# Kernel optimization log

Measured on AMD Instinct MI355X. Metric: run time of the kernel, lower is better.

Reference implementation:

```python
import jax, jax.numpy as jnp
import numpy as np

B, T, C, K, V = 4, 2048, 1024, 1024, 1024
SQRT_K = float(np.sqrt(K))


def setup_inputs() -> dict:
    key = jax.random.key(0)
    ks = jax.random.split(key, 7)
    s = 0.02
    return {
        "x": jax.random.normal(ks[0], (B, T, C), jnp.float32),
        "Wq": (jax.random.normal(ks[1], (C, K), jnp.float32) * s),
        "bq": jnp.zeros((K,), jnp.float32),
        "Wk": (jax.random.normal(ks[2], (C, K), jnp.float32) * s),
        "bk": jnp.zeros((K,), jnp.float32),
        "Wv": (jax.random.normal(ks[3], (C, V), jnp.float32) * s),
        "bv": jnp.zeros((V,), jnp.float32),
    }


def reference(x, Wq, bq, Wk, bk, Wv, bv):
    # projections: [B,T,C] @ [C,K] -> [B,T,K]
    q = x @ Wq + bq
    k = x @ Wk + bk
    v = x @ Wv + bv
    # logits[b,t,s] = q[b,t,:] . k[b,s,:]
    logits = jnp.einsum("btk,bsk->bts", q, k)
    # original mask: mask[j,i] = 1 if i > j -> strict upper triangle masked to -inf
    seq = logits.shape[1]
    mask = jnp.triu(jnp.ones((seq, seq), bool), k=1)
    logits = jnp.where(mask[None, :, :], -jnp.inf, logits)
    # NOTE: original softmax is over dim=1 (query axis), not the key axis
    probs = jax.nn.softmax(logits / SQRT_K, axis=1)
    read = jnp.einsum("bts,bsv->btv", probs, v)
    return jnp.concatenate((x, read), axis=2)
```

## Files before the change

### kernel.cpp

```cpp
#include <hip/hip_runtime.h>
#include <hip/hip_bf16.h>
#include <stdint.h>

#define DEVI __device__ __forceinline__

using u16 = unsigned short;
typedef __attribute__((ext_vector_type(8))) _Float16 halfx8;
typedef __attribute__((ext_vector_type(4))) float f32x4;

constexpr int BB = 4, TT = 2048, CC = 1024, KD = 1024, VD = 1024;
constexpr int QKVW = 3072;
constexpr int OUTW = CC + VD;
constexpr float INV_SQRT_K = 0.03125f;

DEVI u16 f2h(float f) {
  _Float16 h = (_Float16)f;
  return __builtin_bit_cast(u16, h);
}
DEVI float h2f(u16 u) {
  return (float)__builtin_bit_cast(_Float16, u);
}

DEVI void gload16(const u16* g, u16* l) {
  __builtin_amdgcn_global_load_lds(
      (const __attribute__((address_space(1))) void*)g,
      (__attribute__((address_space(3))) void*)l, 16, 0, 0);
}

__global__ void cast_x_copy(const float* __restrict__ x, u16* __restrict__ xh,
                            float* __restrict__ out) {
  size_t i = (size_t)blockIdx.x * blockDim.x + threadIdx.x;
  float4 v = reinterpret_cast<const float4*>(x)[i];
  ushort4 u;
  u.x = f2h(v.x); u.y = f2h(v.y); u.z = f2h(v.z); u.w = f2h(v.w);
  reinterpret_cast<ushort4*>(xh)[i] = u;
  size_t e = i * 4;
  size_t bt = e / CC;
  int c = (int)(e % CC);
  *reinterpret_cast<float4*>(&out[bt * OUTW + c]) = v;
}

__global__ void transpose_cast_w3(const float* __restrict__ Wq,
                                  const float* __restrict__ Wk,
                                  const float* __restrict__ Wv,
                                  u16* __restrict__ Wt) {
  __shared__ float tile[32][33];
  const float* W = (blockIdx.z == 0) ? Wq : (blockIdx.z == 1) ? Wk : Wv;
  u16* dst = Wt + (size_t)blockIdx.z * 1024 * 1024;
  int n0 = blockIdx.x * 32, c0 = blockIdx.y * 32;
  int tx = threadIdx.x, ty = threadIdx.y;
  for (int i = ty; i < 32; i += 8)
    tile[i][tx] = W[(size_t)(c0 + i) * KD + n0 + tx];
  __syncthreads();
  for (int i = ty; i < 32; i += 8)
    dst[(size_t)(n0 + i) * CC + c0 + tx] = f2h(tile[tx][i]);
}

__global__ void concat_bias(const float* __restrict__ bq, const float* __restrict__ bk,
                            const float* __restrict__ bv, float* __restrict__ bc) {
  int n = blockIdx.x * 256 + threadIdx.x;
  float v = (n < 1024) ? bq[n] : (n < 2048) ? bk[n - 1024] : bv[n - 2048];
  bc[n] = v;
}

__global__ void transpose_v(const u16* __restrict__ QKV, const float* __restrict__ Dp,
                            u16* __restrict__ Vt) {
  __shared__ u16 tile[32][33];
  int b = blockIdx.z;
  int n0 = blockIdx.x * 32, s0 = blockIdx.y * 32;
  const u16* src = QKV + (size_t)b * TT * QKVW + 2048;
  u16* dst = Vt + (size_t)b * VD * TT;
  int tx = threadIdx.x, ty = threadIdx.y;
  for (int i = ty; i < 32; i += 8)
    tile[i][tx] = src[(size_t)(s0 + i) * QKVW + n0 + tx];
  const int s = s0 + tx;
  float d = 0.f;
  for (int rt = s >> 8; rt < TT / 256; ++rt)
    d += Dp[((size_t)rt * BB + b) * TT + s];
  float di = 1.f / d;
  __syncthreads();
  for (int i = ty; i < 32; i += 8)
    dst[(size_t)(n0 + i) * TT + s0 + tx] = f2h(h2f(tile[tx][i]) * di);
}

template <typename OutT, int TPB, int BM, int BN, int SWZ, bool CSKIP, bool KLIM,
          bool BIAS, bool CMASK>
__global__ __launch_bounds__(TPB, 2) void gemm_bt(
    const u16* __restrict__ A, const u16* __restrict__ Bm, OutT* __restrict__ Out,
    const float* __restrict__ bias, float* __restrict__ Dp,
    int Kd, int lda, int ldb, int ldo,
    long long strA, long long strB, long long strO, float alpha) {
  constexpr int BK = 32;
  constexpr int WAVES = TPB / 64;
  constexpr int WM = BM / 64, WN = WAVES / WM;
  constexpr int WR = 64, WC = 64;
  constexpr int MR = 4, NR = 4;
  constexpr int RPS = TPB / 4;
  constexpr int SWA = BM / RPS, SWB = BN / RPS;
  constexpr int LPT = SWA + SWB;
  constexpr int ASZ = BM * BK, BSZ = BN * BK;
  __shared__ u16 sA[3 * ASZ];
  __shared__ u16 sB[3 * BSZ];
  __shared__ float reds[CMASK ? WM : 1][CMASK ? BN : 1];

  int bx = blockIdx.x, by = blockIdx.y;
  if constexpr (KLIM) {
    bx = gridDim.x - 1 - bx;
  } else if constexpr (SWZ == 1) {
    const int gx = gridDim.x;
    const int nx = gx >> 3;
    int fid = bx + gx * by;
    int xcd = fid & 7, idx = fid >> 3;
    bx = xcd * nx + idx % nx;
    by = idx / nx;
  }
  const int r0 = bx * BM, c0 = by * BN;
  if (CSKIP && c0 > r0 + BM - 1) return;
  A   += (size_t)blockIdx.z * strA;
  Bm  += (size_t)blockIdx.z * strB;
  Out += (size_t)blockIdx.z * strO;

  const int tid = threadIdx.x;
  const int lane = tid & 63;
  const int w = tid >> 6;
  const int wm = w / WN, wn = w % WN;
  const int l15 = lane & 15, l4 = lane >> 4;
  const int cswz8 = 8 * (l4 ^ ((l15 >> 1) & 3));

  const int srow = tid >> 2;
  const int sc8 = 8 * ((tid & 3) ^ ((tid >> 3) & 3));
  const u16* gA = A + (size_t)(r0 + srow) * lda + sc8;
  const u16* gB = Bm + (size_t)(c0 + srow) * ldb + sc8;
  const int sdst = tid * 8;

  f32x4 acc[MR][NR] = {};

  int kmax = Kd;
  if (KLIM) { int km = r0 + BM; kmax = km < Kd ? km : Kd; }
  const int NT = kmax / BK;

  auto stage = [&](int buf, int kt) {
    const int k0 = kt * BK;
    u16* da = sA + buf * ASZ + sdst;
#pragma unroll
    for (int j = 0; j < SWA; ++j)
      gload16(gA + (size_t)j * RPS * lda + k0, da + j * TPB * 8);
    u16* db = sB + buf * BSZ + sdst;
#pragma unroll
    for (int j = 0; j < SWB; ++j)
      gload16(gB + (size_t)j * RPS * ldb + k0, db + j * TPB * 8);
  };

  stage(0, 0);
  stage(1, 1);
  if constexpr (LPT == 3) asm volatile("s_waitcnt vmcnt(3)" ::: "memory");
  else                    asm volatile("s_waitcnt vmcnt(4)" ::: "memory");
  __builtin_amdgcn_s_barrier();

  int buf = 0;
  for (int kt = 0; kt < NT; ++kt) {
    int nb = buf + 2; if (nb >= 3) nb -= 3;
    const u16* rA = sA + buf * ASZ;
    const u16* rB = sB + buf * BSZ;
    halfx8 af[MR], bfv[NR];
#pragma unroll
    for (int n = 0; n < NR; ++n)
      bfv[n] = *reinterpret_cast<const halfx8*>(&rB[(wn * WC + n * 16 + l15) * BK + cswz8]);
#pragma unroll
    for (int m = 0; m < MR; ++m)
      af[m] = *reinterpret_cast<const halfx8*>(&rA[(wm * WR + m * 16 + l15) * BK + cswz8]);
    if (kt + 2 < NT) stage(nb, kt + 2);
    __builtin_amdgcn_s_setprio(1);
#pragma unroll
    for (int m = 0; m < MR; ++m)
#pragma unroll
      for (int n = 0; n < NR; ++n)
        acc[m][n] = __builtin_amdgcn_mfma_f32_16x16x32_f16(af[m], bfv[n], acc[m][n], 0, 0, 0);
    __builtin_amdgcn_s_setprio(0);
    if (kt + 2 < NT) {
      if constexpr (LPT == 3) asm volatile("s_waitcnt vmcnt(3)" ::: "memory");
      else                    asm volatile("s_waitcnt vmcnt(4)" ::: "memory");
    } else if (kt + 1 < NT) {
      asm volatile("s_waitcnt vmcnt(0)" ::: "memory");
    }
    if (kt + 1 < NT) __builtin_amdgcn_s_barrier();
    buf = buf + 1; if (buf == 3) buf = 0;
  }

  if constexpr (CMASK) {
#pragma unroll
    for (int n = 0; n < NR; ++n) {
      const int gcol = c0 + wn * WC + n * 16 + l15;
      float sm = 0.f;
#pragma unroll
      for (int m = 0; m < MR; ++m) {
        const int growb = r0 + wm * WR + m * 16 + l4 * 4;
#pragma unroll
        for (int r = 0; r < 4; ++r) {
          float p = 0.f;
          if (growb + r >= gcol) p = __expf(acc[m][n][r] * alpha);
          reinterpret_cast<u16*>(Out)[(size_t)(growb + r) * ldo + gcol] = f2h(p);
          sm += p;
        }
      }
      sm += __shfl_xor(sm, 16);
      sm += __shfl_xor(sm, 32);
      if (l4 == 0) reds[wm][wn * WC + n * 16 + l15] = sm;
    }
    __syncthreads();
    if (tid < BN) {
      float d2 = 0.f;
#pragma unroll
      for (int i = 0; i < WM; ++i) d2 += reds[i][tid];
      Dp[((size_t)(r0 >> 8) * BB + blockIdx.z) * TT + c0 + tid] = d2;
    }
  } else {
#pragma unroll
    for (int m = 0; m < MR; ++m) {
      const int growb = r0 + wm * WR + m * 16 + l4 * 4;
#pragma unroll
    for (int n = 0; n < NR; ++n) {
        const int gcol = c0 + wn * WC + n * 16 + l15;
        float bvv = 0.f;
        if (BIAS) bvv = bias[gcol];
#pragma unroll
        for (int r = 0; r < 4; ++r) {
          float val = acc[m][n][r] * alpha + bvv;
          size_t off = (size_t)(growb + r) * ldo + gcol;
          if constexpr (sizeof(OutT) == 2) {
            reinterpret_cast<u16*>(Out)[off] = f2h(val);
          } else {
            reinterpret_cast<float*>(Out)[off] = val;
          }
        }
      }
    }
  }
}

extern "C" void kernel_launch(void* const* d_in, const int* in_sizes, int n_in,
                              void* d_out, int out_size, void* d_ws, size_t ws_size,
                              hipStream_t stream) {
  const float* x  = (const float*)d_in[0];
  const float* Wq = (const float*)d_in[1];
  const float* bq = (const float*)d_in[2];
  const float* Wk = (const float*)d_in[3];
  const float* bk = (const float*)d_in[4];
  const float* Wv = (const float*)d_in[5];
  const float* bv = (const float*)d_in[6];
  float* out = (float*)d_out;
  char* ws = (char*)d_ws;
  constexpr size_t MB = 1024ull * 1024ull;

  u16* xh   = (u16*)(ws);
  u16* QKV  = (u16*)(ws + 16 * MB);
  u16* Wt   = (u16*)(ws + 64 * MB);
  float* bc = (float*)(ws + 70 * MB);
  u16* SP   = (u16*)(ws + 71 * MB);
  u16* Vt = xh;
  float* Dp = (float*)(ws + 64 * MB);

  cast_x_copy<<<dim3((BB * TT * CC / 4) / 256), dim3(256), 0, stream>>>(x, xh, out);
  dim3 tb(32, 8);
  transpose_cast_w3<<<dim3(KD / 32, CC / 32, 3), tb, 0, stream>>>(Wq, Wk, Wv, Wt);
  concat_bias<<<dim3(QKVW / 256), 256, 0, stream>>>(bq, bk, bv, bc);

  gemm_bt<u16, 512, 256, 128, 1, false, false, true, false>
      <<<dim3(32, QKVW / 128, 1), 512, 0, stream>>>(
      xh, Wt, QKV, bc, nullptr, CC, CC, CC, QKVW, 0, 0, 0, 1.f);

  gemm_bt<u16, 512, 256, 128, 0, true, false, false, true>
      <<<dim3(TT / 256, TT / 128, BB), 512, 0, stream>>>(
      QKV, QKV + 1024, SP, nullptr, Dp, KD, QKVW, QKVW, TT,
      (long long)TT * QKVW, (long long)TT * QKVW, (long long)TT * TT, INV_SQRT_K);

  transpose_v<<<dim3(VD / 32, TT / 32, BB), tb, 0, stream>>>(QKV, Dp, Vt);

  gemm_bt<float, 256, 128, 128, 0, false, true, false, false>
      <<<dim3(TT / 128, VD / 128, BB), 256, 0, stream>>>(
      SP, Vt, out + CC, nullptr, nullptr, TT, TT, TT, OUTW,
      (long long)TT * TT, (long long)VD * TT, (long long)TT * OUTW, 1.f);
}
```

Before: 187.1 us.

## Enlarge per-wave GEMM tiles to 128x64 and halve threads per block

Makes the wave tile height a template parameter and sets it to 128 rows, so each wave holds 8x4 MFMA accumulators instead of 4x4. All three GEMMs keep their block tiles but launch with half as many threads. This raises MFMA work per LDS fragment load and reduces LDS read traffic. In exchange it roughly doubles accumulator registers per thread, which can lower occupancy, and each thread issues twice as many global-to-LDS loads per stage, so the vmcnt waits are adjusted to match.

```diff
diff --git a/kernel.cpp b/kernel.cpp
--- a/kernel.cpp
+++ b/kernel.cpp
@@ -83,8 +83,8 @@
     dst[(size_t)(n0 + i) * TT + s0 + tx] = f2h(h2f(tile[tx][i]) * di);
 }
 
-template <typename OutT, int TPB, int BM, int BN, int SWZ, bool CSKIP, bool KLIM,
-          bool BIAS, bool CMASK>
+template <typename OutT, int TPB, int BM, int BN, int WTM, int SWZ, bool CSKIP,
+          bool KLIM, bool BIAS, bool CMASK>
 __global__ __launch_bounds__(TPB, 2) void gemm_bt(
     const u16* __restrict__ A, const u16* __restrict__ Bm, OutT* __restrict__ Out,
     const float* __restrict__ bias, float* __restrict__ Dp,
@@ -92,9 +92,10 @@
     long long strA, long long strB, long long strO, float alpha) {
   constexpr int BK = 32;
   constexpr int WAVES = TPB / 64;
-  constexpr int WM = BM / 64, WN = WAVES / WM;
-  constexpr int WR = 64, WC = 64;
-  constexpr int MR = 4, NR = 4;
+  constexpr int WM = BM / WTM, WN = WAVES / WM;
+  constexpr int WC = BN / WN;
+  static_assert(WC == 64, "wave tile N must be 64");
+  constexpr int MR = WTM / 16, NR = 4;
   constexpr int RPS = TPB / 4;
   constexpr int SWA = BM / RPS, SWB = BN / RPS;
   constexpr int LPT = SWA + SWB;
@@ -151,10 +152,15 @@
       gload16(gB + (size_t)j * RPS * ldb + k0, db + j * TPB * 8);
   };
 
+  auto wait_lpt = [&]() {
+    if constexpr (LPT == 6) asm volatile("s_waitcnt vmcnt(6)" ::: "memory");
+    else if constexpr (LPT == 8) asm volatile("s_waitcnt vmcnt(8)" ::: "memory");
+    else asm volatile("s_waitcnt vmcnt(3)" ::: "memory");
+  };
+
   stage(0, 0);
   stage(1, 1);
-  if constexpr (LPT == 3) asm volatile("s_waitcnt vmcnt(3)" ::: "memory");
-  else                    asm volatile("s_waitcnt vmcnt(4)" ::: "memory");
+  wait_lpt();
   __builtin_amdgcn_s_barrier();
 
   int buf = 0;
@@ -168,7 +174,7 @@
       bfv[n] = *reinterpret_cast<const halfx8*>(&rB[(wn * WC + n * 16 + l15) * BK + cswz8]);
 #pragma unroll
     for (int m = 0; m < MR; ++m)
-      af[m] = *reinterpret_cast<const halfx8*>(&rA[(wm * WR + m * 16 + l15) * BK + cswz8]);
+      af[m] = *reinterpret_cast<const halfx8*>(&rA[(wm * WTM + m * 16 + l15) * BK + cswz8]);
     if (kt + 2 < NT) stage(nb, kt + 2);
     __builtin_amdgcn_s_setprio(1);
 #pragma unroll
@@ -178,8 +184,7 @@
         acc[m][n] = __builtin_amdgcn_mfma_f32_16x16x32_f16(af[m], bfv[n], acc[m][n], 0, 0, 0);
     __builtin_amdgcn_s_setprio(0);
     if (kt + 2 < NT) {
-      if constexpr (LPT == 3) asm volatile("s_waitcnt vmcnt(3)" ::: "memory");
-      else                    asm volatile("s_waitcnt vmcnt(4)" ::: "memory");
+      wait_lpt();
     } else if (kt + 1 < NT) {
       asm volatile("s_waitcnt vmcnt(0)" ::: "memory");
     }
@@ -194,7 +199,7 @@
       float sm = 0.f;
 #pragma unroll
       for (int m = 0; m < MR; ++m) {
-        const int growb = r0 + wm * WR + m * 16 + l4 * 4;
+        const int growb = r0 + wm * WTM + m * 16 + l4 * 4;
 #pragma unroll
         for (int r = 0; r < 4; ++r) {
           float p = 0.f;
@@ -217,9 +222,9 @@
   } else {
 #pragma unroll
     for (int m = 0; m < MR; ++m) {
-      const int growb = r0 + wm * WR + m * 16 + l4 * 4;
-#pragma unroll
-    for (int n = 0; n < NR; ++n) {
+      const int growb = r0 + wm * WTM + m * 16 + l4 * 4;
+#pragma unroll
+      for (int n = 0; n < NR; ++n) {
         const int gcol = c0 + wn * WC + n * 16 + l15;
         float bvv = 0.f;
         if (BIAS) bvv = bias[gcol];
@@ -265,19 +270,19 @@
   transpose_cast_w3<<<dim3(KD / 32, CC / 32, 3), tb, 0, stream>>>(Wq, Wk, Wv, Wt);
   concat_bias<<<dim3(QKVW / 256), 256, 0, stream>>>(bq, bk, bv, bc);
 
-  gemm_bt<u16, 512, 256, 128, 1, false, false, true, false>
-      <<<dim3(32, QKVW / 128, 1), 512, 0, stream>>>(
+  gemm_bt<u16, 256, 256, 128, 128, 1, false, false, true, false>
+      <<<dim3(32, QKVW / 128, 1), 256, 0, stream>>>(
       xh, Wt, QKV, bc, nullptr, CC, CC, CC, QKVW, 0, 0, 0, 1.f);
 
-  gemm_bt<u16, 512, 256, 128, 0, true, false, false, true>
-      <<<dim3(TT / 256, TT / 128, BB), 512, 0, stream>>>(
+  gemm_bt<u16, 256, 256, 128, 128, 0, true, false, false, true>
+      <<<dim3(TT / 256, TT / 128, BB), 256, 0, stream>>>(
       QKV, QKV + 1024, SP, nullptr, Dp, KD, QKVW, QKVW, TT,
       (long long)TT * QKVW, (long long)TT * QKVW, (long long)TT * TT, INV_SQRT_K);
 
   transpose_v<<<dim3(VD / 32, TT / 32, BB), tb, 0, stream>>>(QKV, Dp, Vt);
 
-  gemm_bt<float, 256, 128, 128, 0, false, true, false, false>
-      <<<dim3(TT / 128, VD / 128, BB), 256, 0, stream>>>(
+  gemm_bt<float, 128, 128, 128, 128, 0, false, true, false, false>
+      <<<dim3(TT / 128, VD / 128, BB), 128, 0, stream>>>(
       SP, Vt, out + CC, nullptr, nullptr, TT, TT, TT, OUTW,
       (long long)TT * TT, (long long)VD * TT, (long long)TT * OUTW, 1.f);
 }
```

Result: no change. 188.8 us (+1.0%).
